# Optimization experiments

Hardware: AMD Instinct MI355X
Metric: run time of the kernel (lower is better)

Reference implementation:

```python
import jax, jax.numpy as jnp
import numpy as np

RADIUS = 1.5
PARTITION_NUM = 5
OUT_CHANNEL = 128
IN_CHANNEL = 64
EPS = 1e-5


def setup_inputs() -> dict:
    key = jax.random.key(0)
    ks = jax.random.split(key, 10)
    B, N, npoint, K = 16, 8192, 2048, 32
    D = 61  # points feature dim; in_channel = D + 3 = 64
    xyz = jax.random.normal(ks[0], (B, N, 3), dtype=jnp.float32)
    points = jax.random.normal(ks[1], (B, N, D), dtype=jnp.float32)
    local_coordinates = jax.random.uniform(ks[2], (B, npoint, K, 3), dtype=jnp.float32)
    neighbor_lists = jax.random.randint(ks[3], (B, npoint, K), 0, N)
    data_idx = jax.random.randint(ks[4], (B, npoint), 0, N)
    parameter_list = jnp.zeros((1,), dtype=jnp.float32)
    # params (torch Linear stored transposed here: [in, out])
    W1 = jax.random.normal(ks[5], (IN_CHANNEL * PARTITION_NUM, OUT_CHANNEL), dtype=jnp.float32) * 0.02
    b1 = jnp.zeros((OUT_CHANNEL,), dtype=jnp.float32)
    g1 = jnp.ones((OUT_CHANNEL,), dtype=jnp.float32)
    be1 = jnp.zeros((OUT_CHANNEL,), dtype=jnp.float32)
    W2 = jax.random.normal(ks[6], (OUT_CHANNEL, OUT_CHANNEL), dtype=jnp.float32) * 0.02
    b2 = jnp.zeros((OUT_CHANNEL,), dtype=jnp.float32)
    g2 = jnp.ones((OUT_CHANNEL,), dtype=jnp.float32)
    be2 = jnp.zeros((OUT_CHANNEL,), dtype=jnp.float32)
    return dict(xyz=xyz, points=points, local_coordinates=local_coordinates,
                neighbor_lists=neighbor_lists, parameter_list=parameter_list,
                data_idx=data_idx, W1=W1, b1=b1, g1=g1, be1=be1,
                W2=W2, b2=b2, g2=g2, be2=be2)


def _forward(xyz, points, local_coordinates, parameter_list,
             W1, b1, g1, be1, W2, b2, g2, be2, neighbor_lists, data_idx):
    B, N, _ = xyz.shape
    _, npoint, K = neighbor_lists.shape
    # new_xyz = index_points(xyz, data_idx)
    new_xyz = jnp.take_along_axis(xyz, data_idx[:, :, None], axis=1)  # [B, npoint, 3]
    # points = cat(points, xyz) -> in_channel features
    pts = jnp.concatenate([points, xyz], axis=2)  # [B, N, C]
    C = pts.shape[-1]
    # gather neighbor feats: [B, npoint, K, C] (permute chain in torch is a net identity)
    idx = neighbor_lists.reshape(B, npoint * K)
    grouped = jnp.take_along_axis(pts, idx[:, :, None], axis=1).reshape(B, npoint, K, C)
    # circle_conv: radial binning + scatter-add over partition bins
    lc = local_coordinates.reshape(B, npoint, K, 3)
    dist = jnp.linalg.norm(lc[..., 0:2], axis=-1)          # [B, npoint, K]
    dist = jnp.minimum(dist / RADIUS, 0.99)                # cut(x, 0.99)
    bins = jnp.floor(dist * PARTITION_NUM).astype(jnp.int32)
    onehot = jax.nn.one_hot(bins, PARTITION_NUM, dtype=grouped.dtype)  # [B, npoint, K, P]
    feature = jnp.einsum('bnkp,bnkc->bnpc', onehot, grouped)           # scatter_add
    feature = feature.reshape(B * npoint, PARTITION_NUM * C)
    # Linear + BatchNorm1d (training-mode batch stats) + ReLU
    x = feature @ W1 + b1                                  # [B*npoint, out]
    mu = x.mean(axis=0)
    var = x.var(axis=0)
    x = jax.nn.relu(g1 * (x - mu) / jnp.sqrt(var + EPS) + be1)
    x = x.reshape(B, npoint, -1)
    # Linear + BatchNorm1d over channels + ReLU
    y = x @ W2 + b2                                        # [B, npoint, out]
    mu2 = y.mean(axis=(0, 1))
    var2 = y.var(axis=(0, 1))
    new_points = jax.nn.relu(g2 * (y - mu2) / jnp.sqrt(var2 + EPS) + be2)
    return new_xyz, new_points


def reference(xyz, points, local_coordinates, neighbor_lists, parameter_list,
              data_idx, W1, b1, g1, be1, W2, b2, g2, be2):
    return _forward(xyz, points, local_coordinates, parameter_list,
                    W1, b1, g1, be1, W2, b2, g2, be2, neighbor_lists, data_idx)
```

## Files before the change

kernel.cpp:

```cpp
#include <hip/hip_runtime.h>
#include <hip/hip_bf16.h>
#include <math.h>

#define B_SZ     16
#define N_PTS    8192
#define NPOINT   2048
#define KNBR     32
#define D_FEAT   61
#define C_IN     64
#define P_BINS   5
#define C_OUT    128
#define M_ROWS   (B_SZ * NPOINT)
#define K1       (C_IN * P_BINS)
#define EPSV     1e-5f

typedef __attribute__((ext_vector_type(8))) short bf16x8;
typedef __attribute__((ext_vector_type(4))) float f32x4;

__device__ __forceinline__ unsigned short f2bf_rne(float v) {
    unsigned u = __float_as_uint(v);
    u += 0x7fffu + ((u >> 16) & 1u);
    return (unsigned short)(u >> 16);
}
__device__ __forceinline__ float bf2f(unsigned short v) {
    return __uint_as_float(((unsigned)v) << 16);
}

__device__ __forceinline__ size_t fragB_idx(int n, int c) {
    return ((size_t)((c >> 5) * 8 + (n >> 4)) << 9) +
           ((((c >> 3) & 3) * 16 + (n & 15)) << 3) + (c & 7);
}

__global__ __launch_bounds__(256) void prep_kernel(
    const float* __restrict__ points, const float* __restrict__ xyz,
    const float* __restrict__ W1, const float* __restrict__ W2,
    unsigned short* __restrict__ ptsb, unsigned short* __restrict__ W1f,
    unsigned short* __restrict__ W2f, float* __restrict__ st)
{
    const int blk = blockIdx.x;
    const int tid = threadIdx.x;
    if (blk < 32768) {
        const int xcd  = blk & 7;
        const int slot = blk >> 3;
        const int b    = 2 * xcd + (slot >> 11);
        const int rin  = (slot & 2047) * 4 + (tid >> 6);
        const int row  = b * N_PTS + rin;
        const int c    = tid & 63;
        float v;
        if (c < D_FEAT) v = points[(size_t)row * D_FEAT + c];
        else            v = xyz[(size_t)row * 3 + (c - D_FEAT)];
        ptsb[((size_t)row << 6) | c] = f2bf_rne(v);
    } else {
        const int gid = (blk - 32768) * 256 + tid;
        if (gid < 512) st[gid] = 0.f;
        if (gid < K1 * C_OUT) {
            int c = gid >> 7, n = gid & 127;
            W1f[fragB_idx(n, c)] = f2bf_rne(W1[gid]);
        } else {
            int i = gid - K1 * C_OUT;
            int c = i >> 7, n = i & 127;
            W2f[fragB_idx(n, c)] = f2bf_rne(W2[i]);
        }
    }
}

__global__ __launch_bounds__(256) void gather_kernel(
    const unsigned short* __restrict__ ptsb, const float* __restrict__ xyz,
    const float* __restrict__ lc, const int* __restrict__ nl,
    const int* __restrict__ didx, unsigned short* __restrict__ featf,
    float* __restrict__ newxyz)
{
    const int g    = blockIdx.x;
    const int xcd  = g & 7;
    const int slot = g >> 3;
    const int b    = 2 * xcd + (slot >> 9);
    const int wave = threadIdx.x >> 6;
    const int m    = (slot & 511) * 4 + wave;
    const int bid  = b * NPOINT + m;
    const int lane = threadIdx.x & 63;
    const int k    = lane & 31;

    __shared__ int s_srt[4][32];
    __shared__ __align__(16) unsigned short s_stage[4][32][64];

    const size_t nbase = (size_t)bid * KNBR;
    const float x = lc[(nbase + k) * 3 + 0];
    const float y = lc[(nbase + k) * 3 + 1];
    const float d = fminf(sqrtf(x * x + y * y) * (1.0f / 1.5f), 0.99f);
    int bin = (int)(d * 5.0f);
    bin = bin > 4 ? 4 : (bin < 0 ? 0 : bin);
    const int n = nl[nbase + k];

    unsigned m0 = (unsigned)__ballot(bin == 0);
    unsigned m1 = (unsigned)__ballot(bin == 1);
    unsigned m2 = (unsigned)__ballot(bin == 2);
    unsigned m3 = (unsigned)__ballot(bin == 3);
    unsigned m4 = (unsigned)__ballot(bin == 4);
    const int c0n = __popc(m0), c1n = __popc(m1), c2n = __popc(m2), c3n = __popc(m3);
    const int e0 = c0n, e1 = e0 + c1n, e2 = e1 + c2n, e3 = e2 + c3n;

    int start = (bin > 0 ? c0n : 0) + (bin > 1 ? c1n : 0) +
                (bin > 2 ? c2n : 0) + (bin > 3 ? c3n : 0);
    unsigned mymask = m0;
    mymask = bin == 1 ? m1 : mymask;
    mymask = bin == 2 ? m2 : mymask;
    mymask = bin == 3 ? m3 : mymask;
    mymask = bin == 4 ? m4 : mymask;
    const int pos = start + __popc(mymask & ((1u << k) - 1u));

    if (lane < 32) s_srt[wave][pos] = n;
    if (lane >= 32 && lane < 35) {
        const int di = didx[bid];
        const int j = lane - 32;
        newxyz[(size_t)bid * 3 + j] = xyz[((size_t)b * N_PTS + di) * 3 + j];
    }

    const unsigned short* __restrict__ pb = ptsb + (((size_t)b * N_PTS) << 6);
    const int r = lane >> 3, j7 = lane & 7;
    #pragma unroll
    for (int g4 = 0; g4 < 4; ++g4) {
        const int nr = s_srt[wave][g4 * 8 + r];
        bf16x8 row = *(const bf16x8*)(pb + ((size_t)nr << 6) + j7 * 8);
        *(bf16x8*)&s_stage[wave][g4 * 8 + r][j7 * 8] = row;
    }

    float acc = 0.f, pre0 = 0.f, pre1 = 0.f, pre2 = 0.f, pre3 = 0.f;
    #pragma unroll
    for (int kk = 0; kk < 32; ++kk) {
        acc += bf2f(s_stage[wave][kk][lane]);
        const int kp = kk + 1;
        if (kp == e0) pre0 = acc;
        if (kp == e1) pre1 = acc;
        if (kp == e2) pre2 = acc;
        if (kp == e3) pre3 = acc;
    }
    float vals[5];
    vals[0] = pre0;
    vals[1] = pre1 - pre0;
    vals[2] = pre2 - pre1;
    vals[3] = pre3 - pre2;
    vals[4] = acc - pre3;

    const int t = bid >> 4, lm = bid & 15;
    const int kgl = (lane >> 3) & 3, jl = lane & 7;
    #pragma unroll
    for (int bb = 0; bb < 5; ++bb) {
        const int kb = bb * 2 + (lane >> 5);
        const size_t idx = (((size_t)(t * 10 + kb)) << 9) +
                           ((kgl * 16 + lm) << 3) + jl;
        featf[idx] = f2bf_rne(vals[bb]);
    }
}

__global__ __launch_bounds__(256) void gemm1_mfma(
    const unsigned short* __restrict__ Af, const unsigned short* __restrict__ Wf,
    const float* __restrict__ bias, unsigned short* __restrict__ outf,
    float* __restrict__ sum, float* __restrict__ sumsq)
{
    const int g    = blockIdx.x;
    const int xcd  = g & 7;
    const int slot = g >> 3;
    const int bb_  = 2 * xcd + (slot >> 5);
    const int tile = (bb_ * 32 + (slot & 31)) * 4 + (threadIdx.x >> 6);

    const int tid  = threadIdx.x;
    const int wave = tid >> 6, lane = tid & 63;
    const int lm = lane & 15, kg = lane >> 4;

    f32x4 acc[8] = {};
    #pragma unroll
    for (int kb = 0; kb < 10; ++kb) {
        bf16x8 a = *(const bf16x8*)(Af + (((size_t)(tile * 10 + kb)) << 9) + lane * 8);
        #pragma unroll
        for (int nf = 0; nf < 8; ++nf) {
            bf16x8 bfr = *(const bf16x8*)(Wf + (((size_t)(kb * 8 + nf)) << 9) + lane * 8);
            acc[nf] = __builtin_amdgcn_mfma_f32_16x16x32_bf16(a, bfr, acc[nf], 0, 0, 0);
        }
    }

    __shared__ float s_s[4][128], s_q[4][128];
    #pragma unroll
    for (int nf = 0; nf < 8; ++nf) {
        const int col = nf * 16 + lm;
        const float bb = bias[col];
        float ls = 0.f, lq = 0.f;
        #pragma unroll
        for (int i = 0; i < 4; ++i) {
            float v = acc[nf][i] + bb;
            const size_t idx = (((size_t)(tile * 4 + (col >> 5))) << 9) +
                               ((((col >> 3) & 3) * 16 + kg * 4 + i) << 3) + (col & 7);
            outf[idx] = f2bf_rne(v);
            ls += v; lq += v * v;
        }
        ls += __shfl_xor(ls, 16); ls += __shfl_xor(ls, 32);
        lq += __shfl_xor(lq, 16); lq += __shfl_xor(lq, 32);
        if (kg == 0) { s_s[wave][col] = ls; s_q[wave][col] = lq; }
    }
    __syncthreads();
    if (tid < 128) {
        float ts = s_s[0][tid] + s_s[1][tid] + s_s[2][tid] + s_s[3][tid];
        float tq = s_q[0][tid] + s_q[1][tid] + s_q[2][tid] + s_q[3][tid];
        atomicAdd(&sum[tid], ts);
        atomicAdd(&sumsq[tid], tq);
    }
}

__global__ __launch_bounds__(256) void gemm2_mfma(
    const unsigned short* __restrict__ Xf,
    const float* __restrict__ sum1, const float* __restrict__ sq1,
    const float* __restrict__ g1, const float* __restrict__ be1,
    const unsigned short* __restrict__ Wf, const float* __restrict__ bias,
    unsigned short* __restrict__ out, float* __restrict__ sum,
    float* __restrict__ sumsq)
{
    __shared__ float sc[128], sh[128];
    __shared__ float s_s[4][128], s_q[4][128];
    const int tid = threadIdx.x;
    if (tid < 128) {
        float mu  = sum1[tid] * (1.0f / (float)M_ROWS);
        float var = sq1[tid] * (1.0f / (float)M_ROWS) - mu * mu;
        float iv  = 1.0f / sqrtf(var + EPSV);
        float s   = g1[tid] * iv;
        sc[tid] = s;
        sh[tid] = be1[tid] - mu * s;
    }
    __syncthreads();

    const int g    = blockIdx.x;
    const int xcd  = g & 7;
    const int slot = g >> 3;
    const int bb_  = 2 * xcd + (slot >> 5);
    const int tile = (bb_ * 32 + (slot & 31)) * 4 + (tid >> 6);

    const int wave = tid >> 6, lane = tid & 63;
    const int lm = lane & 15, kg = lane >> 4;

    f32x4 acc[8] = {};
    #pragma unroll
    for (int kb = 0; kb < 4; ++kb) {
        const int c0 = kb * 32 + kg * 8;
        bf16x8 xr = *(const bf16x8*)(Xf + (((size_t)(tile * 4 + kb)) << 9) + lane * 8);
        f32x4 s0 = *(const f32x4*)&sc[c0];
        f32x4 s1 = *(const f32x4*)&sc[c0 + 4];
        f32x4 h0 = *(const f32x4*)&sh[c0];
        f32x4 h1 = *(const f32x4*)&sh[c0 + 4];
        bf16x8 a;
        #pragma unroll
        for (int j = 0; j < 4; ++j) {
            a[j]     = (short)f2bf_rne(fmaxf(0.f, s0[j] * bf2f((unsigned short)xr[j]) + h0[j]));
            a[4 + j] = (short)f2bf_rne(fmaxf(0.f, s1[j] * bf2f((unsigned short)xr[4 + j]) + h1[j]));
        }
        #pragma unroll
        for (int nf = 0; nf < 8; ++nf) {
            bf16x8 bfr = *(const bf16x8*)(Wf + (((size_t)(kb * 8 + nf)) << 9) + lane * 8);
            acc[nf] = __builtin_amdgcn_mfma_f32_16x16x32_bf16(a, bfr, acc[nf], 0, 0, 0);
        }
    }

    const int orow = tile * 16 + kg * 4;
    #pragma unroll
    for (int nf = 0; nf < 8; ++nf) {
        const int col = nf * 16 + lm;
        const float bb = bias[col];
        float ls = 0.f, lq = 0.f;
        #pragma unroll
        for (int i = 0; i < 4; ++i) {
            float v = acc[nf][i] + bb;
            out[(size_t)(orow + i) * C_OUT + col] = f2bf_rne(v);
            ls += v; lq += v * v;
        }
        ls += __shfl_xor(ls, 16); ls += __shfl_xor(ls, 32);
        lq += __shfl_xor(lq, 16); lq += __shfl_xor(lq, 32);
        if (kg == 0) { s_s[wave][col] = ls; s_q[wave][col] = lq; }
    }
    __syncthreads();
    if (tid < 128) {
        float ts = s_s[0][tid] + s_s[1][tid] + s_s[2][tid] + s_s[3][tid];
        float tq = s_q[0][tid] + s_q[1][tid] + s_q[2][tid] + s_q[3][tid];
        atomicAdd(&sum[tid], ts);
        atomicAdd(&sumsq[tid], tq);
    }
}

__global__ __launch_bounds__(256) void out_kernel(
    const unsigned short* __restrict__ Y,
    const float* __restrict__ sum2, const float* __restrict__ sq2,
    const float* __restrict__ g2, const float* __restrict__ be2,
    float* __restrict__ out)
{
    __shared__ float sc[128], sh[128];
    const int tid = threadIdx.x;
    if (tid < 128) {
        float mu  = sum2[tid] * (1.0f / (float)M_ROWS);
        float var = sq2[tid] * (1.0f / (float)M_ROWS) - mu * mu;
        float iv  = 1.0f / sqrtf(var + EPSV);
        float s   = g2[tid] * iv;
        sc[tid] = s;
        sh[tid] = be2[tid] - mu * s;
    }
    __syncthreads();

    const size_t e8 = (size_t)blockIdx.x * 256 + tid;
    bf16x8 v = ((const bf16x8*)Y)[e8];
    const int cb = (int)((e8 * 8) & 127);
    float4 r0, r1;
    r0.x = fmaxf(0.f, sc[cb + 0] * bf2f((unsigned short)v[0]) + sh[cb + 0]);
    r0.y = fmaxf(0.f, sc[cb + 1] * bf2f((unsigned short)v[1]) + sh[cb + 1]);
    r0.z = fmaxf(0.f, sc[cb + 2] * bf2f((unsigned short)v[2]) + sh[cb + 2]);
    r0.w = fmaxf(0.f, sc[cb + 3] * bf2f((unsigned short)v[3]) + sh[cb + 3]);
    r1.x = fmaxf(0.f, sc[cb + 4] * bf2f((unsigned short)v[4]) + sh[cb + 4]);
    r1.y = fmaxf(0.f, sc[cb + 5] * bf2f((unsigned short)v[5]) + sh[cb + 5]);
    r1.z = fmaxf(0.f, sc[cb + 6] * bf2f((unsigned short)v[6]) + sh[cb + 6]);
    r1.w = fmaxf(0.f, sc[cb + 7] * bf2f((unsigned short)v[7]) + sh[cb + 7]);
    ((float4*)out)[e8 * 2]     = r0;
    ((float4*)out)[e8 * 2 + 1] = r1;
}

extern "C" void kernel_launch(void* const* d_in, const int* in_sizes, int n_in,
                              void* d_out, int out_size, void* d_ws, size_t ws_size,
                              hipStream_t stream)
{
    const float* xyz    = (const float*)d_in[0];
    const float* points = (const float*)d_in[1];
    const float* lc     = (const float*)d_in[2];
    const int*   nl     = (const int*)d_in[3];
    const int*   didx   = (const int*)d_in[5];
    const float* W1     = (const float*)d_in[6];
    const float* b1     = (const float*)d_in[7];
    const float* g1     = (const float*)d_in[8];
    const float* be1    = (const float*)d_in[9];
    const float* W2     = (const float*)d_in[10];
    const float* b2     = (const float*)d_in[11];
    const float* g2     = (const float*)d_in[12];
    const float* be2    = (const float*)d_in[13];

    float* out = (float*)d_out;
    char*  ws  = (char*)d_ws;

    unsigned short* ptsb  = (unsigned short*)ws;
    unsigned short* x1f   = (unsigned short*)ws;
    unsigned short* yb    = (unsigned short*)(ws + 8388608);
    unsigned short* featf = (unsigned short*)(ws + 16777216);
    unsigned short* W1f   = (unsigned short*)(ws + 37748736);
    unsigned short* W2f   = (unsigned short*)(ws + 37830656);
    float*          st    = (float*)(ws + 37863424);

    prep_kernel<<<32768 + 224, 256, 0, stream>>>(points, xyz, W1, W2,
                                                 ptsb, W1f, W2f, st);
    gather_kernel<<<M_ROWS / 4, 256, 0, stream>>>(ptsb, xyz, lc, nl, didx, featf, out);
    gemm1_mfma<<<M_ROWS / 64, 256, 0, stream>>>(featf, W1f, b1, x1f, st, st + 128);
    gemm2_mfma<<<M_ROWS / 64, 256, 0, stream>>>(x1f, st, st + 128, g1, be1,
                                                W2f, b2, yb, st + 256, st + 384);
    out_kernel<<<(M_ROWS * C_OUT) / (256 * 8), 256, 0, stream>>>(
        yb, st + 256, st + 384, g2, be2, out + (size_t)M_ROWS * 3);
}
```

Before: 200.1 us.

## Fuse neighbor gather and binning into GEMM1, drop bf16 points pre-pass

Removes the pass that converted the whole points+xyz tensor to bf16 and merges the gather/partition-sum kernel with the first MFMA GEMM. The binned feature tile now stays in shared memory instead of round-tripping through global memory. Neighbor rows are read straight from the fp32 inputs with per-lane scalar loads. BN statistics are accumulated into 8 XCD-replicated slots, which later kernels reduce, to cut atomic contention. The trade-off is narrower, less coalesced fp32 gathers, more work per block and smaller 16-row GEMM tiles that reload W1 fragments per block.

```diff
diff --git a/kernel.cpp b/kernel.cpp
--- a/kernel.cpp
+++ b/kernel.cpp
@@ -32,197 +32,176 @@
 }
 
 __global__ __launch_bounds__(256) void prep_kernel(
-    const float* __restrict__ points, const float* __restrict__ xyz,
     const float* __restrict__ W1, const float* __restrict__ W2,
-    unsigned short* __restrict__ ptsb, unsigned short* __restrict__ W1f,
-    unsigned short* __restrict__ W2f, float* __restrict__ st)
-{
-    const int blk = blockIdx.x;
-    const int tid = threadIdx.x;
-    if (blk < 32768) {
-        const int xcd  = blk & 7;
-        const int slot = blk >> 3;
-        const int b    = 2 * xcd + (slot >> 11);
-        const int rin  = (slot & 2047) * 4 + (tid >> 6);
-        const int row  = b * N_PTS + rin;
-        const int c    = tid & 63;
-        float v;
-        if (c < D_FEAT) v = points[(size_t)row * D_FEAT + c];
-        else            v = xyz[(size_t)row * 3 + (c - D_FEAT)];
-        ptsb[((size_t)row << 6) | c] = f2bf_rne(v);
-    } else {
-        const int gid = (blk - 32768) * 256 + tid;
-        if (gid < 512) st[gid] = 0.f;
-        if (gid < K1 * C_OUT) {
-            int c = gid >> 7, n = gid & 127;
-            W1f[fragB_idx(n, c)] = f2bf_rne(W1[gid]);
-        } else {
-            int i = gid - K1 * C_OUT;
-            int c = i >> 7, n = i & 127;
-            W2f[fragB_idx(n, c)] = f2bf_rne(W2[i]);
-        }
-    }
-}
-
-__global__ __launch_bounds__(256) void gather_kernel(
-    const unsigned short* __restrict__ ptsb, const float* __restrict__ xyz,
+    unsigned short* __restrict__ W1f, unsigned short* __restrict__ W2f,
+    float* __restrict__ st)
+{
+    const int gid = blockIdx.x * 256 + threadIdx.x;
+    if (gid < 40960) {
+        int c = gid >> 7, n = gid & 127;
+        W1f[fragB_idx(n, c)] = f2bf_rne(W1[gid]);
+    } else if (gid < 57344) {
+        int i = gid - 40960;
+        int c = i >> 7, n = i & 127;
+        W2f[fragB_idx(n, c)] = f2bf_rne(W2[i]);
+    } else if (gid < 61440) {
+        st[gid - 57344] = 0.f;
+    }
+}
+
+__global__ __launch_bounds__(256) void fusedg1_kernel(
+    const float* __restrict__ xyz, const float* __restrict__ points,
     const float* __restrict__ lc, const int* __restrict__ nl,
-    const int* __restrict__ didx, unsigned short* __restrict__ featf,
-    float* __restrict__ newxyz)
+    const int* __restrict__ didx, const unsigned short* __restrict__ W1f,
+    const float* __restrict__ b1, unsigned short* __restrict__ x1f,
+    float* __restrict__ st, float* __restrict__ newxyz)
 {
     const int g    = blockIdx.x;
     const int xcd  = g & 7;
     const int slot = g >> 3;
-    const int b    = 2 * xcd + (slot >> 9);
+    const int b    = 2 * xcd + (slot >> 7);
+    const int t16  = slot & 127;
+    const int tile = b * 128 + t16;
     const int wave = threadIdx.x >> 6;
-    const int m    = (slot & 511) * 4 + wave;
-    const int bid  = b * NPOINT + m;
     const int lane = threadIdx.x & 63;
     const int k    = lane & 31;
+    const int lm   = lane & 15, kg = lane >> 4;
+    const int kgl  = (lane >> 3) & 3, jl = lane & 7, khalf = lane >> 5;
 
     __shared__ int s_srt[4][32];
-    __shared__ __align__(16) unsigned short s_stage[4][32][64];
-
-    const size_t nbase = (size_t)bid * KNBR;
-    const float x = lc[(nbase + k) * 3 + 0];
-    const float y = lc[(nbase + k) * 3 + 1];
-    const float d = fminf(sqrtf(x * x + y * y) * (1.0f / 1.5f), 0.99f);
-    int bin = (int)(d * 5.0f);
-    bin = bin > 4 ? 4 : (bin < 0 ? 0 : bin);
-    const int n = nl[nbase + k];
-
-    unsigned m0 = (unsigned)__ballot(bin == 0);
-    unsigned m1 = (unsigned)__ballot(bin == 1);
-    unsigned m2 = (unsigned)__ballot(bin == 2);
-    unsigned m3 = (unsigned)__ballot(bin == 3);
-    unsigned m4 = (unsigned)__ballot(bin == 4);
-    const int c0n = __popc(m0), c1n = __popc(m1), c2n = __popc(m2), c3n = __popc(m3);
-    const int e0 = c0n, e1 = e0 + c1n, e2 = e1 + c2n, e3 = e2 + c3n;
-
-    int start = (bin > 0 ? c0n : 0) + (bin > 1 ? c1n : 0) +
-                (bin > 2 ? c2n : 0) + (bin > 3 ? c3n : 0);
-    unsigned mymask = m0;
-    mymask = bin == 1 ? m1 : mymask;
-    mymask = bin == 2 ? m2 : mymask;
-    mymask = bin == 3 ? m3 : mymask;
-    mymask = bin == 4 ? m4 : mymask;
-    const int pos = start + __popc(mymask & ((1u << k) - 1u));
-
-    if (lane < 32) s_srt[wave][pos] = n;
-    if (lane >= 32 && lane < 35) {
-        const int di = didx[bid];
-        const int j = lane - 32;
-        newxyz[(size_t)bid * 3 + j] = xyz[((size_t)b * N_PTS + di) * 3 + j];
-    }
-
-    const unsigned short* __restrict__ pb = ptsb + (((size_t)b * N_PTS) << 6);
-    const int r = lane >> 3, j7 = lane & 7;
-    #pragma unroll
-    for (int g4 = 0; g4 < 4; ++g4) {
-        const int nr = s_srt[wave][g4 * 8 + r];
-        bf16x8 row = *(const bf16x8*)(pb + ((size_t)nr << 6) + j7 * 8);
-        *(bf16x8*)&s_stage[wave][g4 * 8 + r][j7 * 8] = row;
-    }
-
-    float acc = 0.f, pre0 = 0.f, pre1 = 0.f, pre2 = 0.f, pre3 = 0.f;
-    #pragma unroll
-    for (int kk = 0; kk < 32; ++kk) {
-        acc += bf2f(s_stage[wave][kk][lane]);
-        const int kp = kk + 1;
-        if (kp == e0) pre0 = acc;
-        if (kp == e1) pre1 = acc;
-        if (kp == e2) pre2 = acc;
-        if (kp == e3) pre3 = acc;
-    }
-    float vals[5];
-    vals[0] = pre0;
-    vals[1] = pre1 - pre0;
-    vals[2] = pre2 - pre1;
-    vals[3] = pre3 - pre2;
-    vals[4] = acc - pre3;
-
-    const int t = bid >> 4, lm = bid & 15;
-    const int kgl = (lane >> 3) & 3, jl = lane & 7;
-    #pragma unroll
-    for (int bb = 0; bb < 5; ++bb) {
-        const int kb = bb * 2 + (lane >> 5);
-        const size_t idx = (((size_t)(t * 10 + kb)) << 9) +
-                           ((kgl * 16 + lm) << 3) + jl;
-        featf[idx] = f2bf_rne(vals[bb]);
-    }
-}
-
-__global__ __launch_bounds__(256) void gemm1_mfma(
-    const unsigned short* __restrict__ Af, const unsigned short* __restrict__ Wf,
-    const float* __restrict__ bias, unsigned short* __restrict__ outf,
-    float* __restrict__ sum, float* __restrict__ sumsq)
-{
-    const int g    = blockIdx.x;
-    const int xcd  = g & 7;
-    const int slot = g >> 3;
-    const int bb_  = 2 * xcd + (slot >> 5);
-    const int tile = (bb_ * 32 + (slot & 31)) * 4 + (threadIdx.x >> 6);
-
-    const int tid  = threadIdx.x;
-    const int wave = tid >> 6, lane = tid & 63;
-    const int lm = lane & 15, kg = lane >> 4;
-
-    f32x4 acc[8] = {};
+    __shared__ __align__(16) unsigned short sA[10 * 512];
+
+    const float* __restrict__ pbase = points + (size_t)b * N_PTS * D_FEAT;
+    const float* __restrict__ xbase = xyz + (size_t)b * N_PTS * 3;
+
+    for (int p = 0; p < 4; ++p) {
+        const int mloc = wave * 4 + p;
+        const int bid  = tile * 16 + mloc;
+        const size_t nbase = (size_t)bid * KNBR;
+
+        const float x = lc[(nbase + k) * 3 + 0];
+        const float y = lc[(nbase + k) * 3 + 1];
+        const float dd = fminf(sqrtf(x * x + y * y) * (1.0f / 1.5f), 0.99f);
+        int bin = (int)(dd * 5.0f);
+        bin = bin > 4 ? 4 : (bin < 0 ? 0 : bin);
+        const int n = nl[nbase + k];
+
+        unsigned m0 = (unsigned)__ballot(bin == 0);
+        unsigned m1 = (unsigned)__ballot(bin == 1);
+        unsigned m2 = (unsigned)__ballot(bin == 2);
+        unsigned m3 = (unsigned)__ballot(bin == 3);
+        unsigned m4 = (unsigned)__ballot(bin == 4);
+        const int c0n = __popc(m0), c1n = __popc(m1);
+        const int c2n = __popc(m2), c3n = __popc(m3);
+        const int e0 = c0n, e1 = e0 + c1n, e2 = e1 + c2n, e3 = e2 + c3n;
+
+        int start = (bin > 0 ? c0n : 0) + (bin > 1 ? c1n : 0) +
+                    (bin > 2 ? c2n : 0) + (bin > 3 ? c3n : 0);
+        unsigned mymask = m0;
+        mymask = bin == 1 ? m1 : mymask;
+        mymask = bin == 2 ? m2 : mymask;
+        mymask = bin == 3 ? m3 : mymask;
+        mymask = bin == 4 ? m4 : mymask;
+        const int pos = start + __popc(mymask & ((1u << k) - 1u));
+
+        if (lane < 32) s_srt[wave][pos] = n;
+        if (lane >= 32 && lane < 35) {
+            const int di = didx[bid];
+            newxyz[(size_t)bid * 3 + (lane - 32)] = xbase[(size_t)di * 3 + (lane - 32)];
+        }
+
+        float v[32];
+        #pragma unroll
+        for (int kk = 0; kk < 32; ++kk) {
+            const int nr = __builtin_amdgcn_readfirstlane(s_srt[wave][kk]);
+            float t;
+            if (lane < D_FEAT) t = pbase[nr * D_FEAT + lane];
+            else               t = xbase[nr * 3 + (lane - D_FEAT)];
+            v[kk] = t;
+        }
+
+        float acc = 0.f, pre0 = 0.f, pre1 = 0.f, pre2 = 0.f, pre3 = 0.f;
+        #pragma unroll
+        for (int kk = 0; kk < 32; ++kk) {
+            acc += v[kk];
+            const int kp = kk + 1;
+            if (kp == e0) pre0 = acc;
+            if (kp == e1) pre1 = acc;
+            if (kp == e2) pre2 = acc;
+            if (kp == e3) pre3 = acc;
+        }
+        float vals[5];
+        vals[0] = pre0;
+        vals[1] = pre1 - pre0;
+        vals[2] = pre2 - pre1;
+        vals[3] = pre3 - pre2;
+        vals[4] = acc - pre3;
+
+        #pragma unroll
+        for (int bb = 0; bb < 5; ++bb) {
+            const int kb = bb * 2 + khalf;
+            sA[kb * 512 + (kgl * 16 + mloc) * 8 + jl] = f2bf_rne(vals[bb]);
+        }
+    }
+    __syncthreads();
+
+    f32x4 acc0 = {}, acc1 = {};
     #pragma unroll
     for (int kb = 0; kb < 10; ++kb) {
-        bf16x8 a = *(const bf16x8*)(Af + (((size_t)(tile * 10 + kb)) << 9) + lane * 8);
-        #pragma unroll
-        for (int nf = 0; nf < 8; ++nf) {
-            bf16x8 bfr = *(const bf16x8*)(Wf + (((size_t)(kb * 8 + nf)) << 9) + lane * 8);
-            acc[nf] = __builtin_amdgcn_mfma_f32_16x16x32_bf16(a, bfr, acc[nf], 0, 0, 0);
-        }
-    }
-
-    __shared__ float s_s[4][128], s_q[4][128];
+        bf16x8 a = *(const bf16x8*)&sA[kb * 512 + lane * 8];
+        bf16x8 w0 = *(const bf16x8*)(W1f + ((size_t)(kb * 8 + wave * 2) << 9) + lane * 8);
+        bf16x8 w1 = *(const bf16x8*)(W1f + ((size_t)(kb * 8 + wave * 2 + 1) << 9) + lane * 8);
+        acc0 = __builtin_amdgcn_mfma_f32_16x16x32_bf16(a, w0, acc0, 0, 0, 0);
+        acc1 = __builtin_amdgcn_mfma_f32_16x16x32_bf16(a, w1, acc1, 0, 0, 0);
+    }
+
+    const int rep = (g & 7) * 128;
     #pragma unroll
-    for (int nf = 0; nf < 8; ++nf) {
-        const int col = nf * 16 + lm;
-        const float bb = bias[col];
+    for (int q = 0; q < 2; ++q) {
+        const f32x4 A = q ? acc1 : acc0;
+        const int col = (wave * 2 + q) * 16 + lm;
+        const float bb = b1[col];
         float ls = 0.f, lq = 0.f;
         #pragma unroll
         for (int i = 0; i < 4; ++i) {
-            float v = acc[nf][i] + bb;
+            float vv = A[i] + bb;
             const size_t idx = (((size_t)(tile * 4 + (col >> 5))) << 9) +
                                ((((col >> 3) & 3) * 16 + kg * 4 + i) << 3) + (col & 7);
-            outf[idx] = f2bf_rne(v);
-            ls += v; lq += v * v;
+            x1f[idx] = f2bf_rne(vv);
+            ls += vv; lq += vv * vv;
         }
         ls += __shfl_xor(ls, 16); ls += __shfl_xor(ls, 32);
         lq += __shfl_xor(lq, 16); lq += __shfl_xor(lq, 32);
-        if (kg == 0) { s_s[wave][col] = ls; s_q[wave][col] = lq; }
-    }
-    __syncthreads();
-    if (tid < 128) {
-        float ts = s_s[0][tid] + s_s[1][tid] + s_s[2][tid] + s_s[3][tid];
-        float tq = s_q[0][tid] + s_q[1][tid] + s_q[2][tid] + s_q[3][tid];
-        atomicAdd(&sum[tid], ts);
-        atomicAdd(&sumsq[tid], tq);
+        if (kg == 0) {
+            atomicAdd(&st[rep + col], ls);
+            atomicAdd(&st[1024 + rep + col], lq);
+        }
     }
 }
 
 __global__ __launch_bounds__(256) void gemm2_mfma(
     const unsigned short* __restrict__ Xf,
-    const float* __restrict__ sum1, const float* __restrict__ sq1,
+    const float* __restrict__ st_in,
     const float* __restrict__ g1, const float* __restrict__ be1,
     const unsigned short* __restrict__ Wf, const float* __restrict__ bias,
-    unsigned short* __restrict__ out, float* __restrict__ sum,
-    float* __restrict__ sumsq)
+    unsigned short* __restrict__ out, float* __restrict__ st)
 {
     __shared__ float sc[128], sh[128];
     __shared__ float s_s[4][128], s_q[4][128];
     const int tid = threadIdx.x;
     if (tid < 128) {
-        float mu  = sum1[tid] * (1.0f / (float)M_ROWS);
-        float var = sq1[tid] * (1.0f / (float)M_ROWS) - mu * mu;
+        float s = 0.f, q = 0.f;
+        #pragma unroll
+        for (int r = 0; r < 8; ++r) {
+            s += st_in[r * 128 + tid];
+            q += st_in[1024 + r * 128 + tid];
+        }
+        float mu  = s * (1.0f / (float)M_ROWS);
+        float var = q * (1.0f / (float)M_ROWS) - mu * mu;
         float iv  = 1.0f / sqrtf(var + EPSV);
-        float s   = g1[tid] * iv;
-        sc[tid] = s;
-        sh[tid] = be1[tid] - mu * s;
+        float sg  = g1[tid] * iv;
+        sc[tid] = sg;
+        sh[tid] = be1[tid] - mu * sg;
     }
     __syncthreads();
 
@@ -275,28 +254,34 @@
     }
     __syncthreads();
     if (tid < 128) {
+        const int rep = (g & 7) * 128;
         float ts = s_s[0][tid] + s_s[1][tid] + s_s[2][tid] + s_s[3][tid];
         float tq = s_q[0][tid] + s_q[1][tid] + s_q[2][tid] + s_q[3][tid];
-        atomicAdd(&sum[tid], ts);
-        atomicAdd(&sumsq[tid], tq);
+        atomicAdd(&st[2048 + rep + tid], ts);
+        atomicAdd(&st[3072 + rep + tid], tq);
     }
 }
 
 __global__ __launch_bounds__(256) void out_kernel(
-    const unsigned short* __restrict__ Y,
-    const float* __restrict__ sum2, const float* __restrict__ sq2,
+    const unsigned short* __restrict__ Y, const float* __restrict__ st,
     const float* __restrict__ g2, const float* __restrict__ be2,
     float* __restrict__ out)
 {
     __shared__ float sc[128], sh[128];
     const int tid = threadIdx.x;
     if (tid < 128) {
-        float mu  = sum2[tid] * (1.0f / (float)M_ROWS);
-        float var = sq2[tid] * (1.0f / (float)M_ROWS) - mu * mu;
+        float s = 0.f, q = 0.f;
+        #pragma unroll
+        for (int r = 0; r < 8; ++r) {
+            s += st[2048 + r * 128 + tid];
+            q += st[3072 + r * 128 + tid];
+        }
+        float mu  = s * (1.0f / (float)M_ROWS);
+        float var = q * (1.0f / (float)M_ROWS) - mu * mu;
         float iv  = 1.0f / sqrtf(var + EPSV);
-        float s   = g2[tid] * iv;
-        sc[tid] = s;
-        sh[tid] = be2[tid] - mu * s;
+        float sg  = g2[tid] * iv;
+        sc[tid] = sg;
+        sh[tid] = be2[tid] - mu * sg;
     }
     __syncthreads();
 
@@ -337,20 +322,17 @@
     float* out = (float*)d_out;
     char*  ws  = (char*)d_ws;
 
-    unsigned short* ptsb  = (unsigned short*)ws;
-    unsigned short* x1f   = (unsigned short*)ws;
-    unsigned short* yb    = (unsigned short*)(ws + 8388608);
-    unsigned short* featf = (unsigned short*)(ws + 16777216);
-    unsigned short* W1f   = (unsigned short*)(ws + 37748736);
-    unsigned short* W2f   = (unsigned short*)(ws + 37830656);
-    float*          st    = (float*)(ws + 37863424);
-
-    prep_kernel<<<32768 + 224, 256, 0, stream>>>(points, xyz, W1, W2,
-                                                 ptsb, W1f, W2f, st);
-    gather_kernel<<<M_ROWS / 4, 256, 0, stream>>>(ptsb, xyz, lc, nl, didx, featf, out);
-    gemm1_mfma<<<M_ROWS / 64, 256, 0, stream>>>(featf, W1f, b1, x1f, st, st + 128);
-    gemm2_mfma<<<M_ROWS / 64, 256, 0, stream>>>(x1f, st, st + 128, g1, be1,
-                                                W2f, b2, yb, st + 256, st + 384);
+    unsigned short* x1f = (unsigned short*)ws;
+    unsigned short* yb  = (unsigned short*)(ws + 8388608);
+    unsigned short* W1f = (unsigned short*)(ws + 16777216);
+    unsigned short* W2f = (unsigned short*)(ws + 16859136);
+    float*          st  = (float*)(ws + 16891904);
+
+    prep_kernel<<<240, 256, 0, stream>>>(W1, W2, W1f, W2f, st);
+    fusedg1_kernel<<<M_ROWS / 16, 256, 0, stream>>>(xyz, points, lc, nl, didx,
+                                                    W1f, b1, x1f, st, out);
+    gemm2_mfma<<<M_ROWS / 64, 256, 0, stream>>>(x1f, st, g1, be1,
+                                                W2f, b2, yb, st);
     out_kernel<<<(M_ROWS * C_OUT) / (256 * 8), 256, 0, stream>>>(
-        yb, st + 256, st + 384, g2, be2, out + (size_t)M_ROWS * 3);
-}
+        yb, st, g2, be2, out + (size_t)M_ROWS * 3);
+}
```

Measured after the change: 168.4 us. 15.8% less time.
